# Performance work log

Hardware: AMD Instinct MI355X
Metric: run time of the kernel (lower is better)

Reference implementation:

```python
import jax, jax.numpy as jnp
import numpy as np
import math

B, L, D, H, FF = 4, 1024, 1024, 16, 4096
DH = D // H
EPS = 1e-12


def layer_norm(x, gamma, beta):
    mean = x.mean(-1, keepdims=True)
    var = ((x - mean) ** 2).mean(-1, keepdims=True)  # biased var, matches unbiased=False
    return gamma * (x - mean) / jnp.sqrt(var + EPS) + beta


def setup_inputs() -> dict:
    key = jax.random.key(0)
    ks = jax.random.split(key, 16)
    s = 0.02
    return {
        "x": jax.random.normal(ks[0], (B, L, D), jnp.float32),
        "attn_bias": jax.random.uniform(ks[1], (B, L, L), jnp.float32),
        "src_mask": jax.random.randint(ks[2], (B, L), 0, 2, jnp.int32),
        "wq": jax.random.normal(ks[3], (D, D), jnp.float32) * s,
        "bq": jnp.zeros((D,), jnp.float32),
        "wk": jax.random.normal(ks[4], (D, D), jnp.float32) * s,
        "bk": jnp.zeros((D,), jnp.float32),
        "wv": jax.random.normal(ks[5], (D, D), jnp.float32) * s,
        "bv": jnp.zeros((D,), jnp.float32),
        "wo": jax.random.normal(ks[6], (D, D), jnp.float32) * s,
        "bo": jnp.zeros((D,), jnp.float32),
        "gamma1": jnp.ones((D,), jnp.float32),
        "beta1": jnp.zeros((D,), jnp.float32),
        "w1": jax.random.normal(ks[7], (D, FF), jnp.float32) * s,
        "b1": jnp.zeros((FF,), jnp.float32),
        "w2": jax.random.normal(ks[8], (FF, D), jnp.float32) * s,
        "b2": jnp.zeros((D,), jnp.float32),
        "gamma2": jnp.ones((D,), jnp.float32),
        "beta2": jnp.zeros((D,), jnp.float32),
    }


def reference(x, attn_bias, src_mask, wq, bq, wk, bk, wv, bv, wo, bo,
              gamma1, beta1, w1, b1, w2, b2, gamma2, beta2):
    # ---- multi-head attention with multiplicative bias + additive mask ----
    def split_heads(t):  # [B,L,D] -> [B,H,L,DH]
        return t.reshape(B, L, H, DH).transpose(0, 2, 1, 3)

    q = split_heads(x @ wq + bq)
    k = split_heads(x @ wk + bk)
    v = split_heads(x @ wv + bv)

    score = jnp.einsum('bhqd,bhkd->bhqk', q, k) / math.sqrt(DH)
    score = score * attn_bias[:, None, :, :]               # multiplicative bias
    score = jnp.where(src_mask[:, None, None, :] == 0, -10000.0, score)
    p = jax.nn.softmax(score, axis=-1)
    ctx = jnp.einsum('bhqk,bhkd->bhqd', p, v)
    ctx = ctx.transpose(0, 2, 1, 3).reshape(B, L, D)
    attn_out = ctx @ wo + bo

    h = layer_norm(x + attn_out, gamma1, beta1)

    # ---- position-wise FFN ----
    ffn = jax.nn.relu(h @ w1 + b1) @ w2 + b2
    out = layer_norm(h + ffn, gamma2, beta2)
    return out
```

## Files before the change

kernel.cpp:

```cpp
#include <hip/hip_runtime.h>
#include <hip/hip_bf16.h>
#include <math.h>

#define BB 4
#define LL 1024
#define DD 1024
#define HH 16
#define DHH 64
#define FFF 4096
#define MM (BB*LL)
#define LDQ 3072

typedef __attribute__((ext_vector_type(8))) short short8;
typedef __attribute__((ext_vector_type(4))) float f32x4;

__device__ __forceinline__ ushort f2bf(float f) {
    __hip_bfloat16 h = __float2bfloat16(f);
    return *(ushort*)&h;
}
__device__ __forceinline__ float bf2f(ushort u) {
    __hip_bfloat16 h = *(__hip_bfloat16*)&u;
    return __bfloat162float(h);
}
__device__ __forceinline__ float fexp2(float x) {
#if __has_builtin(__builtin_amdgcn_exp2f)
    return __builtin_amdgcn_exp2f(x);
#else
    return exp2f(x);
#endif
}

__device__ __forceinline__ float block_reduce_sum(float v, float* red, int tid) {
    red[tid] = v;
    __syncthreads();
    for (int off = 128; off > 0; off >>= 1) {
        if (tid < off) red[tid] += red[tid + off];
        __syncthreads();
    }
    float r = red[0];
    __syncthreads();
    return r;
}

__global__ __launch_bounds__(256)
void cast_bf16(const float* __restrict__ in, ushort* __restrict__ out) {
    const int i = blockIdx.x * 256 + threadIdx.x;
    float4 v = ((const float4*)in)[i];
    ushort4 o;
    o.x = f2bf(v.x); o.y = f2bf(v.y); o.z = f2bf(v.z); o.w = f2bf(v.w);
    ((ushort4*)out)[i] = o;
}

__global__ __launch_bounds__(256)
void swizzle_bias(const float* __restrict__ bias, ushort* __restrict__ B) {
    __shared__ float rowbuf[1024];
    const int row = blockIdx.x;
    const int t = threadIdx.x;
    *(float4*)&rowbuf[t * 4] = *(const float4*)&bias[(size_t)row * 1024 + t * 4];
    __syncthreads();
    const int kt = t >> 4, c = t & 15;
    const float s = 1.4426950408889634f;
    ushort4 o;
    o.x = f2bf(rowbuf[kt * 64 + 0 * 16 + c] * s);
    o.y = f2bf(rowbuf[kt * 64 + 1 * 16 + c] * s);
    o.z = f2bf(rowbuf[kt * 64 + 2 * 16 + c] * s);
    o.w = f2bf(rowbuf[kt * 64 + 3 * 16 + c] * s);
    *(ushort4*)&B[(size_t)row * 1024 + t * 4] = o;
}

__global__ __launch_bounds__(256)
void transpose_cast(const float* __restrict__ W, ushort* __restrict__ WT,
                    int K, int N) {
    __shared__ float tile[32][33];
    const int n0 = blockIdx.x * 32, k0 = blockIdx.y * 32;
    const int t = threadIdx.x;
    const int r = t >> 3, c4 = (t & 7) * 4;
    float4 v = *(const float4*)&W[(size_t)(k0 + r) * N + n0 + c4];
    tile[r][c4 + 0] = v.x; tile[r][c4 + 1] = v.y;
    tile[r][c4 + 2] = v.z; tile[r][c4 + 3] = v.w;
    __syncthreads();
    ushort4 o;
    o.x = f2bf(tile[c4 + 0][r]);
    o.y = f2bf(tile[c4 + 1][r]);
    o.z = f2bf(tile[c4 + 2][r]);
    o.w = f2bf(tile[c4 + 3][r]);
    *(ushort4*)&WT[(size_t)(n0 + r) * K + k0 + c4] = o;
}

__global__ __launch_bounds__(256)
void concat3(const float* __restrict__ a, const float* __restrict__ b,
             const float* __restrict__ c, float* __restrict__ o) {
    const int i = blockIdx.x * 256 + threadIdx.x;
    o[i] = (i < 1024) ? a[i] : ((i < 2048) ? b[i - 1024] : c[i - 2048]);
}

template<int BN>
__global__ __launch_bounds__(256)
void gemm_bf16(const ushort* __restrict__ A, const ushort* __restrict__ Bt,
               const float* __restrict__ bias, void* __restrict__ C,
               ushort* __restrict__ Vt, int vn0,
               int M, int N, int K, int relu, int obf16, int qlim) {
    constexpr int JF = BN / 32;
    __shared__ ushort Als0[128 * 32];
    __shared__ ushort Als1[128 * 32];
    __shared__ ushort Bls0[BN * 32];
    __shared__ ushort Bls1[BN * 32];

    const int L = blockIdx.x + gridDim.x * blockIdx.y;
    const int xcd = L & 7;
    const int idx = L >> 3;
    const int mpx = gridDim.y >> 3;
    const int bm = (xcd * mpx + (idx % mpx)) * 128;
    const int bn = (idx / mpx) * BN;

    const int t = threadIdx.x;
    const int lane = t & 63;
    const int w = t >> 6;
    const int wm = (w >> 1) * 64;
    const int wn = (w & 1) * (BN / 2);
    const int fm = lane & 15;
    const int kg = lane >> 4;

    f32x4 acc[4][JF] = {};

    for (int k0 = 0; k0 < K; k0 += 64) {
        #pragma unroll
        for (int j = 0; j < 2; ++j) {
            const int chunk = j * 256 + t;
            const int row = chunk >> 2, kc = chunk & 3;
            const ushort* ga0 = A + (size_t)(bm + row) * K + k0 + kc * 8;
            __builtin_amdgcn_global_load_lds(
                (const __attribute__((address_space(1))) void*)ga0,
                (__attribute__((address_space(3))) void*)(Als0 + chunk * 8), 16, 0, 0);
            const ushort* ga1 = ga0 + 32;
            __builtin_amdgcn_global_load_lds(
                (const __attribute__((address_space(1))) void*)ga1,
                (__attribute__((address_space(3))) void*)(Als1 + chunk * 8), 16, 0, 0);
        }
        #pragma unroll
        for (int j = 0; j < BN / 64; ++j) {
            const int chunk = j * 256 + t;
            const int row = chunk >> 2, kc = chunk & 3;
            const ushort* gb0 = Bt + (size_t)(bn + row) * K + k0 + kc * 8;
            __builtin_amdgcn_global_load_lds(
                (const __attribute__((address_space(1))) void*)gb0,
                (__attribute__((address_space(3))) void*)(Bls0 + chunk * 8), 16, 0, 0);
            const ushort* gb1 = gb0 + 32;
            __builtin_amdgcn_global_load_lds(
                (const __attribute__((address_space(1))) void*)gb1,
                (__attribute__((address_space(3))) void*)(Bls1 + chunk * 8), 16, 0, 0);
        }
        __syncthreads();

        short8 af[4][2], bfr[JF][2];
        #pragma unroll
        for (int i = 0; i < 4; ++i) {
            af[i][0] = *(const short8*)&Als0[(wm + i * 16 + fm) * 32 + kg * 8];
            af[i][1] = *(const short8*)&Als1[(wm + i * 16 + fm) * 32 + kg * 8];
        }
        #pragma unroll
        for (int j = 0; j < JF; ++j) {
            bfr[j][0] = *(const short8*)&Bls0[(wn + j * 16 + fm) * 32 + kg * 8];
            bfr[j][1] = *(const short8*)&Bls1[(wn + j * 16 + fm) * 32 + kg * 8];
        }
        #pragma unroll
        for (int i = 0; i < 4; ++i)
            #pragma unroll
            for (int j = 0; j < JF; ++j) {
                acc[i][j] = __builtin_amdgcn_mfma_f32_16x16x32_bf16(
                    af[i][0], bfr[j][0], acc[i][j], 0, 0, 0);
                acc[i][j] = __builtin_amdgcn_mfma_f32_16x16x32_bf16(
                    af[i][1], bfr[j][1], acc[i][j], 0, 0, 0);
            }
        __syncthreads();
    }

    const int orow0 = (lane >> 4) * 4;
    const int ocol = lane & 15;
    #pragma unroll
    for (int j = 0; j < JF; ++j) {
        const int n = bn + wn + j * 16 + ocol;
        const float bv = bias[n];
        const bool isV = (bn + wn + j * 16) >= vn0;
        #pragma unroll
        for (int i = 0; i < 4; ++i) {
            const int m0 = bm + wm + i * 16 + orow0;
            if (isV) {
                ushort4 o;
                float v0 = acc[i][j][0] + bv, v1 = acc[i][j][1] + bv;
                float v2 = acc[i][j][2] + bv, v3 = acc[i][j][3] + bv;
                o.x = f2bf(v0); o.y = f2bf(v1); o.z = f2bf(v2); o.w = f2bf(v3);
                *(ushort4*)&Vt[((size_t)((m0 >> 10) << 10) + (n - vn0)) * 1024 + (m0 & 1023)] = o;
            } else {
                #pragma unroll
                for (int r = 0; r < 4; ++r) {
                    const int m = m0 + r;
                    float v = acc[i][j][r] + bv;
                    if (relu) v = fmaxf(v, 0.0f);
                    if (n < qlim) v *= 0.125f;
                    if (obf16)
                        ((ushort*)C)[(size_t)m * N + n] = f2bf(v);
                    else
                        ((float*)C)[(size_t)m * N + n] = v;
                }
            }
        }
    }
}

__global__ __launch_bounds__(256, 3)
void attn_mfma(const ushort* __restrict__ QKVb, const ushort* __restrict__ Vt,
               const ushort* __restrict__ biasw, const int* __restrict__ mask,
               ushort* __restrict__ ctx) {
    const int q0 = blockIdx.x * 64;
    const int h = blockIdx.y;
    const int b = blockIdx.z;
    const int t = threadIdx.x;
    const int lane = t & 63;
    const int w = t >> 6;
    const int g = lane >> 4;
    const int c = lane & 15;

    __shared__ ushort QP[64 * 72];
    __shared__ ushort Ks[64 * 72];
    __shared__ ushort Vs[64 * 72];
    __shared__ int maskS[LL];

    #pragma unroll
    for (int i = 0; i < 2; ++i) {
        const int chunk = i * 256 + t;
        const int row = chunk >> 3, c8 = (chunk & 7) * 8;
        *(short8*)&QP[row * 72 + c8] =
            *(const short8*)(QKVb + ((size_t)(b * LL + q0 + row)) * LDQ + h * DHH + c8);
    }
    ((int4*)maskS)[t] = ((const int4*)(mask + b * LL))[t];

    short8 pk[2], pv[2];
    #pragma unroll
    for (int i = 0; i < 2; ++i) {
        const int chunk = i * 256 + t;
        const int row = chunk >> 3, c8 = (chunk & 7) * 8;
        pk[i] = *(const short8*)(QKVb + ((size_t)(b * LL + row)) * LDQ + 1024 + h * DHH + c8);
        pv[i] = *(const short8*)(Vt + ((size_t)((b * HH + h) * DHH + row)) * LL + c8);
    }
    __syncthreads();

    short8 aq0 = *(const short8*)&QP[(w * 16 + c) * 72 + g * 8];
    short8 aq1 = *(const short8*)&QP[(w * 16 + c) * 72 + g * 8 + 32];
    ushort* Pw = QP + w * (16 * 72);

    float m_pr[4] = {-3.4e38f, -3.4e38f, -3.4e38f, -3.4e38f};
    float l_run[4] = {0.f, 0.f, 0.f, 0.f};
    f32x4 acc_o[4] = {};

    for (int kt = 0; kt < 16; ++kt) {
        #pragma unroll
        for (int i = 0; i < 2; ++i) {
            const int chunk = i * 256 + t;
            const int row = chunk >> 3, c8 = (chunk & 7) * 8;
            *(short8*)&Ks[row * 72 + c8] = pk[i];
            *(short8*)&Vs[row * 72 + c8] = pv[i];
        }
        __syncthreads();

        if (kt < 15) {
            const int k0n = (kt + 1) * 64;
            #pragma unroll
            for (int i = 0; i < 2; ++i) {
                const int chunk = i * 256 + t;
                const int row = chunk >> 3, c8 = (chunk & 7) * 8;
                pk[i] = *(const short8*)(QKVb + ((size_t)(b * LL + k0n + row)) * LDQ + 1024 + h * DHH + c8);
                pv[i] = *(const short8*)(Vt + ((size_t)((b * HH + h) * DHH + row)) * LL + k0n + c8);
            }
        }

        ushort4 pb[4];
        #pragma unroll
        for (int r = 0; r < 4; ++r) {
            const int q = q0 + w * 16 + 4 * g + r;
            pb[r] = *(const ushort4*)&biasw[((size_t)(b * LL + q) * 16 + kt) * 64 + c * 4];
        }
        int mk[4];
        #pragma unroll
        for (int j = 0; j < 4; ++j) mk[j] = maskS[kt * 64 + j * 16 + c];

        f32x4 accs[4] = {};
        #pragma unroll
        for (int j = 0; j < 4; ++j) {
            short8 bk0 = *(const short8*)&Ks[(j * 16 + c) * 72 + g * 8];
            short8 bk1 = *(const short8*)&Ks[(j * 16 + c) * 72 + g * 8 + 32];
            accs[j] = __builtin_amdgcn_mfma_f32_16x16x32_bf16(aq0, bk0, accs[j], 0, 0, 0);
            accs[j] = __builtin_amdgcn_mfma_f32_16x16x32_bf16(aq1, bk1, accs[j], 0, 0, 0);
        }

        float sc[4][4];
        #pragma unroll
        for (int j = 0; j < 4; ++j)
            #pragma unroll
            for (int r = 0; r < 4; ++r) {
                const float bw = bf2f(((const ushort*)&pb[r])[j]);
                const float v = accs[j][r] * bw;
                sc[j][r] = (mk[j] == 0) ? -14427.0f : v;
            }

        float mt[4];
        #pragma unroll
        for (int r = 0; r < 4; ++r)
            mt[r] = fmaxf(fmaxf(sc[0][r], sc[1][r]), fmaxf(sc[2][r], sc[3][r]));
        #pragma unroll
        for (int d = 1; d < 16; d <<= 1)
            #pragma unroll
            for (int r = 0; r < 4; ++r)
                mt[r] = fmaxf(mt[r], __shfl_xor(mt[r], d));

        float al[4], lt[4];
        #pragma unroll
        for (int r = 0; r < 4; ++r) {
            const float mn = fmaxf(m_pr[r], mt[r]);
            al[r] = fexp2(m_pr[r] - mn);
            m_pr[r] = mn;
            lt[r] = 0.0f;
        }

        #pragma unroll
        for (int j = 0; j < 4; ++j)
            #pragma unroll
            for (int r = 0; r < 4; ++r) {
                const float pe = fexp2(sc[j][r] - m_pr[r]);
                lt[r] += pe;
                Pw[(4 * g + r) * 72 + j * 16 + c] = f2bf(pe);
            }

        const bool ones = (al[0] == 1.0f) & (al[1] == 1.0f) &
                          (al[2] == 1.0f) & (al[3] == 1.0f);
        if (!__all(ones)) {
            #pragma unroll
            for (int r = 0; r < 4; ++r) l_run[r] *= al[r];
            #pragma unroll
            for (int j = 0; j < 4; ++j)
                #pragma unroll
                for (int r = 0; r < 4; ++r)
                    acc_o[j][r] *= al[r];
        }
        #pragma unroll
        for (int r = 0; r < 4; ++r) l_run[r] += lt[r];

        #pragma unroll
        for (int ks = 0; ks < 2; ++ks) {
            short8 ap = *(const short8*)&Pw[c * 72 + ks * 32 + g * 8];
            #pragma unroll
            for (int j = 0; j < 4; ++j) {
                short8 bv8 = *(const short8*)&Vs[(j * 16 + c) * 72 + ks * 32 + g * 8];
                acc_o[j] = __builtin_amdgcn_mfma_f32_16x16x32_bf16(ap, bv8, acc_o[j], 0, 0, 0);
            }
        }
        __syncthreads();
    }

    #pragma unroll
    for (int r = 0; r < 4; ++r) {
        float l = l_run[r];
        #pragma unroll
        for (int d = 1; d < 16; d <<= 1) l += __shfl_xor(l, d);
        const float inv = 1.0f / l;
        #pragma unroll
        for (int j = 0; j < 4; ++j)
            ctx[((size_t)(b * LL + q0 + w * 16 + 4 * g + r)) * DD + h * DHH + j * 16 + c] =
                f2bf(acc_o[j][r] * inv);
    }
}

__global__ __launch_bounds__(256)
void add_ln_kernel(const float* __restrict__ a, const float* __restrict__ bres,
                   const float* __restrict__ gamma, const float* __restrict__ beta,
                   float* __restrict__ out, ushort* __restrict__ outb) {
    const int row = blockIdx.x;
    const int tid = threadIdx.x;
    __shared__ float red[256];

    const size_t base = (size_t)row * DD;
    float v[4];
    float sum = 0.0f;
    #pragma unroll
    for (int i = 0; i < 4; ++i) {
        const int col = tid + i * 256;
        v[i] = a[base + col] + bres[base + col];
        sum += v[i];
    }
    const float mean = block_reduce_sum(sum, red, tid) * (1.0f / 1024.0f);
    float vs = 0.0f;
    #pragma unroll
    for (int i = 0; i < 4; ++i) {
        const float dlt = v[i] - mean;
        vs += dlt * dlt;
    }
    const float var = block_reduce_sum(vs, red, tid) * (1.0f / 1024.0f);
    const float rstd = rsqrtf(var + 1e-12f);
    #pragma unroll
    for (int i = 0; i < 4; ++i) {
        const int col = tid + i * 256;
        const float o = gamma[col] * (v[i] - mean) * rstd + beta[col];
        out[base + col] = o;
        if (outb) outb[base + col] = f2bf(o);
    }
}

extern "C" void kernel_launch(void* const* d_in, const int* in_sizes, int n_in,
                              void* d_out, int out_size, void* d_ws, size_t ws_size,
                              hipStream_t stream) {
    const float* x         = (const float*)d_in[0];
    const float* attn_bias = (const float*)d_in[1];
    const int*   src_mask  = (const int*)  d_in[2];
    const float* wq = (const float*)d_in[3];
    const float* bq = (const float*)d_in[4];
    const float* wk = (const float*)d_in[5];
    const float* bk = (const float*)d_in[6];
    const float* wv = (const float*)d_in[7];
    const float* bv = (const float*)d_in[8];
    const float* wo = (const float*)d_in[9];
    const float* bo = (const float*)d_in[10];
    const float* gamma1 = (const float*)d_in[11];
    const float* beta1  = (const float*)d_in[12];
    const float* w1 = (const float*)d_in[13];
    const float* b1 = (const float*)d_in[14];
    const float* w2 = (const float*)d_in[15];
    const float* b2 = (const float*)d_in[16];
    const float* gamma2 = (const float*)d_in[17];
    const float* beta2  = (const float*)d_in[18];
    float* out = (float*)d_out;

    const size_t MB = 1024 * 1024;
    char* W = (char*)d_ws;
    ushort* xb    = (ushort*)(W + 0);
    ushort* ctxb  = (ushort*)(W + 0);
    ushort* QKVb  = (ushort*)(W + 8 * MB);
    ushort* F1b   = (ushort*)(W + 8 * MB);
    ushort* Vt    = (ushort*)(W + 40 * MB);
    ushort* W1T   = (ushort*)(W + 40 * MB);
    ushort* WQKVT = (ushort*)(W + 48 * MB);
    ushort* WOT   = (ushort*)(W + 48 * MB);
    ushort* Hbb   = (ushort*)(W + 54 * MB);
    ushort* W2T   = (ushort*)(W + 54 * MB);
    float*  bqkv  = (float*) (W + 62 * MB);
    ushort* biasw = (ushort*)(W + 64 * MB);
    float*  Ao    = (float*) (W + 64 * MB);
    float*  F2    = (float*) (W + 64 * MB);
    float*  Hb    = (float*) (W + 80 * MB);

    dim3 blk(256);

    cast_bf16<<<dim3(4096), blk, 0, stream>>>(x, xb);
    swizzle_bias<<<dim3(4096), blk, 0, stream>>>(attn_bias, biasw);
    transpose_cast<<<dim3(32, 32), blk, 0, stream>>>(wq, WQKVT, DD, DD);
    transpose_cast<<<dim3(32, 32), blk, 0, stream>>>(wk, WQKVT + 1024 * 1024, DD, DD);
    transpose_cast<<<dim3(32, 32), blk, 0, stream>>>(wv, WQKVT + 2048 * 1024, DD, DD);
    concat3<<<dim3(12), blk, 0, stream>>>(bq, bk, bv, bqkv);
    gemm_bf16<128><<<dim3(24, 32), blk, 0, stream>>>(xb, WQKVT, bqkv, QKVb,
                                                     Vt, 2048, MM, LDQ, DD, 0, 1, 1024);
    attn_mfma<<<dim3(16, HH, BB), blk, 0, stream>>>(QKVb, Vt, biasw, src_mask, ctxb);
    transpose_cast<<<dim3(32, 32), blk, 0, stream>>>(wo, WOT, DD, DD);
    gemm_bf16<64><<<dim3(16, 32), blk, 0, stream>>>(ctxb, WOT, bo, Ao,
                                                    Vt, 1 << 30, MM, DD, DD, 0, 0, 0);
    add_ln_kernel<<<dim3(MM), blk, 0, stream>>>(Ao, x, gamma1, beta1, Hb, Hbb);
    transpose_cast<<<dim3(128, 32), blk, 0, stream>>>(w1, W1T, DD, FFF);
    gemm_bf16<128><<<dim3(32, 32), blk, 0, stream>>>(Hbb, W1T, b1, F1b,
                                                     Vt, 1 << 30, MM, FFF, DD, 1, 1, 0);
    transpose_cast<<<dim3(32, 128), blk, 0, stream>>>(w2, W2T, FFF, DD);
    gemm_bf16<64><<<dim3(16, 32), blk, 0, stream>>>(F1b, W2T, b2, F2,
                                                    Vt, 1 << 30, MM, DD, FFF, 0, 0, 0);
    add_ln_kernel<<<dim3(MM), blk, 0, stream>>>(F2, Hb, gamma2, beta2, out, nullptr);
}
```

Measured before the change: 400.6 us.

## Split-K the N=1024 output GEMMs and fold the partial reduction into add+LayerNorm

Adds a split-K GEMM kernel that divides K into two halves across blockIdx.z and writes two fp32 partial products. The following add+LayerNorm kernel now sums both partials plus the bias and the residual, so no extra reduction kernel is needed. The goal is to double the block count for the Wo and W2 GEMMs, which had only 512 blocks with N=1024, and so fill the GPU better. The cost is writing and reading an extra fp32 M×N buffer, and the workspace layout is reshuffled to make room.

New measurement: 397.5 us. About the same (-0.8%).

```diff
diff --git a/kernel.cpp b/kernel.cpp
--- a/kernel.cpp
+++ b/kernel.cpp
@@ -208,6 +208,103 @@
     }
 }
 
+template<int BN>
+__global__ __launch_bounds__(256)
+void gemm_bf16_sk(const ushort* __restrict__ A, const ushort* __restrict__ Bt,
+                  float* __restrict__ P, int M, int N, int K) {
+    constexpr int JF = BN / 32;
+    __shared__ ushort Als0[128 * 32];
+    __shared__ ushort Als1[128 * 32];
+    __shared__ ushort Bls0[BN * 32];
+    __shared__ ushort Bls1[BN * 32];
+
+    const int L = blockIdx.x + gridDim.x * blockIdx.y;
+    const int xcd = L & 7;
+    const int idx = L >> 3;
+    const int mpx = gridDim.y >> 3;
+    const int bm = (xcd * mpx + (idx % mpx)) * 128;
+    const int bn = (idx / mpx) * BN;
+    const int kbeg = blockIdx.z * (K >> 1);
+    const int kend = kbeg + (K >> 1);
+
+    const int t = threadIdx.x;
+    const int lane = t & 63;
+    const int w = t >> 6;
+    const int wm = (w >> 1) * 64;
+    const int wn = (w & 1) * (BN / 2);
+    const int fm = lane & 15;
+    const int kg = lane >> 4;
+
+    f32x4 acc[4][JF] = {};
+
+    for (int k0 = kbeg; k0 < kend; k0 += 64) {
+        #pragma unroll
+        for (int j = 0; j < 2; ++j) {
+            const int chunk = j * 256 + t;
+            const int row = chunk >> 2, kc = chunk & 3;
+            const ushort* ga0 = A + (size_t)(bm + row) * K + k0 + kc * 8;
+            __builtin_amdgcn_global_load_lds(
+                (const __attribute__((address_space(1))) void*)ga0,
+                (__attribute__((address_space(3))) void*)(Als0 + chunk * 8), 16, 0, 0);
+            const ushort* ga1 = ga0 + 32;
+            __builtin_amdgcn_global_load_lds(
+                (const __attribute__((address_space(1))) void*)ga1,
+                (__attribute__((address_space(3))) void*)(Als1 + chunk * 8), 16, 0, 0);
+        }
+        #pragma unroll
+        for (int j = 0; j < BN / 64; ++j) {
+            const int chunk = j * 256 + t;
+            const int row = chunk >> 2, kc = chunk & 3;
+            const ushort* gb0 = Bt + (size_t)(bn + row) * K + k0 + kc * 8;
+            __builtin_amdgcn_global_load_lds(
+                (const __attribute__((address_space(1))) void*)gb0,
+                (__attribute__((address_space(3))) void*)(Bls0 + chunk * 8), 16, 0, 0);
+            const ushort* gb1 = gb0 + 32;
+            __builtin_amdgcn_global_load_lds(
+                (const __attribute__((address_space(1))) void*)gb1,
+                (__attribute__((address_space(3))) void*)(Bls1 + chunk * 8), 16, 0, 0);
+        }
+        __syncthreads();
+
+        short8 af[4][2], bfr[JF][2];
+        #pragma unroll
+        for (int i = 0; i < 4; ++i) {
+            af[i][0] = *(const short8*)&Als0[(wm + i * 16 + fm) * 32 + kg * 8];
+            af[i][1] = *(const short8*)&Als1[(wm + i * 16 + fm) * 32 + kg * 8];
+        }
+        #pragma unroll
+        for (int j = 0; j < JF; ++j) {
+            bfr[j][0] = *(const short8*)&Bls0[(wn + j * 16 + fm) * 32 + kg * 8];
+            bfr[j][1] = *(const short8*)&Bls1[(wn + j * 16 + fm) * 32 + kg * 8];
+        }
+        #pragma unroll
+        for (int i = 0; i < 4; ++i)
+            #pragma unroll
+            for (int j = 0; j < JF; ++j) {
+                acc[i][j] = __builtin_amdgcn_mfma_f32_16x16x32_bf16(
+                    af[i][0], bfr[j][0], acc[i][j], 0, 0, 0);
+                acc[i][j] = __builtin_amdgcn_mfma_f32_16x16x32_bf16(
+                    af[i][1], bfr[j][1], acc[i][j], 0, 0, 0);
+            }
+        __syncthreads();
+    }
+
+    float* Pz = P + (size_t)blockIdx.z * M * N;
+    const int orow0 = (lane >> 4) * 4;
+    const int ocol = lane & 15;
+    #pragma unroll
+    for (int j = 0; j < JF; ++j) {
+        const int n = bn + wn + j * 16 + ocol;
+        #pragma unroll
+        for (int i = 0; i < 4; ++i) {
+            const int m0 = bm + wm + i * 16 + orow0;
+            #pragma unroll
+            for (int r = 0; r < 4; ++r)
+                Pz[(size_t)(m0 + r) * N + n] = acc[i][j][r];
+        }
+    }
+}
+
 __global__ __launch_bounds__(256, 3)
 void attn_mfma(const ushort* __restrict__ QKVb, const ushort* __restrict__ Vt,
                const ushort* __restrict__ biasw, const int* __restrict__ mask,
@@ -371,7 +468,8 @@
 }
 
 __global__ __launch_bounds__(256)
-void add_ln_kernel(const float* __restrict__ a, const float* __restrict__ bres,
+void add_ln_kernel(const float* __restrict__ P0, const float* __restrict__ P1,
+                   const float* __restrict__ cb, const float* __restrict__ bres,
                    const float* __restrict__ gamma, const float* __restrict__ beta,
                    float* __restrict__ out, ushort* __restrict__ outb) {
     const int row = blockIdx.x;
@@ -384,7 +482,7 @@
     #pragma unroll
     for (int i = 0; i < 4; ++i) {
         const int col = tid + i * 256;
-        v[i] = a[base + col] + bres[base + col];
+        v[i] = P0[base + col] + P1[base + col] + cb[col] + bres[base + col];
         sum += v[i];
     }
     const float mean = block_reduce_sum(sum, red, tid) * (1.0f / 1024.0f);
@@ -433,19 +531,18 @@
     char* W = (char*)d_ws;
     ushort* xb    = (ushort*)(W + 0);
     ushort* ctxb  = (ushort*)(W + 0);
+    ushort* W1T   = (ushort*)(W + 0);
     ushort* QKVb  = (ushort*)(W + 8 * MB);
-    ushort* F1b   = (ushort*)(W + 8 * MB);
+    float*  Hb    = (float*) (W + 8 * MB);
+    ushort* Hbb   = (ushort*)(W + 24 * MB);
+    ushort* W2T   = (ushort*)(W + 24 * MB);
+    ushort* F1b   = (ushort*)(W + 32 * MB);
     ushort* Vt    = (ushort*)(W + 40 * MB);
-    ushort* W1T   = (ushort*)(W + 40 * MB);
     ushort* WQKVT = (ushort*)(W + 48 * MB);
     ushort* WOT   = (ushort*)(W + 48 * MB);
-    ushort* Hbb   = (ushort*)(W + 54 * MB);
-    ushort* W2T   = (ushort*)(W + 54 * MB);
     float*  bqkv  = (float*) (W + 62 * MB);
     ushort* biasw = (ushort*)(W + 64 * MB);
-    float*  Ao    = (float*) (W + 64 * MB);
-    float*  F2    = (float*) (W + 64 * MB);
-    float*  Hb    = (float*) (W + 80 * MB);
+    float*  P0    = (float*) (W + 64 * MB);
 
     dim3 blk(256);
 
@@ -459,14 +556,14 @@
                                                      Vt, 2048, MM, LDQ, DD, 0, 1, 1024);
     attn_mfma<<<dim3(16, HH, BB), blk, 0, stream>>>(QKVb, Vt, biasw, src_mask, ctxb);
     transpose_cast<<<dim3(32, 32), blk, 0, stream>>>(wo, WOT, DD, DD);
-    gemm_bf16<64><<<dim3(16, 32), blk, 0, stream>>>(ctxb, WOT, bo, Ao,
-                                                    Vt, 1 << 30, MM, DD, DD, 0, 0, 0);
-    add_ln_kernel<<<dim3(MM), blk, 0, stream>>>(Ao, x, gamma1, beta1, Hb, Hbb);
+    gemm_bf16_sk<64><<<dim3(16, 32, 2), blk, 0, stream>>>(ctxb, WOT, P0, MM, DD, DD);
     transpose_cast<<<dim3(128, 32), blk, 0, stream>>>(w1, W1T, DD, FFF);
+    add_ln_kernel<<<dim3(MM), blk, 0, stream>>>(P0, P0 + (size_t)MM * DD, bo, x,
+                                                gamma1, beta1, Hb, Hbb);
     gemm_bf16<128><<<dim3(32, 32), blk, 0, stream>>>(Hbb, W1T, b1, F1b,
                                                      Vt, 1 << 30, MM, FFF, DD, 1, 1, 0);
     transpose_cast<<<dim3(32, 128), blk, 0, stream>>>(w2, W2T, FFF, DD);
-    gemm_bf16<64><<<dim3(16, 32), blk, 0, stream>>>(F1b, W2T, b2, F2,
-                                                    Vt, 1 << 30, MM, DD, FFF, 0, 0, 0);
-    add_ln_kernel<<<dim3(MM), blk, 0, stream>>>(F2, Hb, gamma2, beta2, out, nullptr);
-}
+    gemm_bf16_sk<64><<<dim3(16, 32, 2), blk, 0, stream>>>(F1b, W2T, P0, MM, DD, FFF);
+    add_ln_kernel<<<dim3(MM), blk, 0, stream>>>(P0, P0 + (size_t)MM * DD, b2, Hb,
+                                                gamma2, beta2, out, nullptr);
+}
```
